# Performance work log

Measured on AMD Instinct MI355X. Metric: run time of the kernel, lower is better.

Reference implementation:

```python
import jax, jax.numpy as jnp
import numpy as np

N_EMBD = 1024
N_HEAD = 16
HEAD_DIM = N_EMBD // N_HEAD


def setup_inputs() -> dict:
    key = jax.random.key(0)
    ks = jax.random.split(key, 9)
    B, T, C = 2, 2048, N_EMBD
    s = 1.0 / np.sqrt(C)
    inp = {
        "x": jax.random.normal(ks[0], (B, T, C), dtype=jnp.float32),
        "Wq": jax.random.normal(ks[1], (C, C), dtype=jnp.float32) * s,
        "bq": jnp.zeros((C,), dtype=jnp.float32),
        "Wk": jax.random.normal(ks[2], (C, C), dtype=jnp.float32) * s,
        "bk": jnp.zeros((C,), dtype=jnp.float32),
        "Wv": jax.random.normal(ks[3], (C, C), dtype=jnp.float32) * s,
        "bv": jnp.zeros((C,), dtype=jnp.float32),
        "Wo": jax.random.normal(ks[4], (C, C), dtype=jnp.float32) * s,
        "bo": jnp.zeros((C,), dtype=jnp.float32),
    }
    return inp


def reference(x, Wq, bq, Wk, bk, Wv, bv, Wo, bo):
    B, T, C = x.shape
    H, D = N_HEAD, HEAD_DIM
    # projections (torch Linear: x @ W^T + b)
    q = (x @ Wq.T + bq).reshape(B, T, H, D).transpose(0, 2, 1, 3)  # [B,H,T,D]
    k = (x @ Wk.T + bk).reshape(B, T, H, D).transpose(0, 2, 1, 3)
    v = (x @ Wv.T + bv).reshape(B, T, H, D).transpose(0, 2, 1, 3)
    scores = jnp.einsum("bhqd,bhkd->bhqk", q, k) / jnp.sqrt(jnp.asarray(D, x.dtype))
    causal = jnp.tril(jnp.ones((T, T), dtype=bool))
    scores = jnp.where(causal[None, None], scores, jnp.asarray(-jnp.inf, x.dtype))
    weights = jax.nn.softmax(scores, axis=-1)  # [B,H,T,T]
    attended = jnp.einsum("bhqk,bhkd->bhqd", weights, v)
    attended = attended.transpose(0, 2, 1, 3).reshape(B, T, C)
    return attended @ Wo.T + bo
```

## Files before the change

kernel.cpp:

```cpp
#include <hip/hip_runtime.h>

typedef unsigned short u16;
typedef __attribute__((ext_vector_type(8))) __bf16 bf16x8;
typedef __attribute__((ext_vector_type(4))) float f32x4;
typedef __attribute__((ext_vector_type(4))) unsigned int u32x4;

#define MFMA16(a, b, c) __builtin_amdgcn_mfma_f32_16x16x32_bf16(a, b, c, 0, 0, 0)

__device__ __forceinline__ u16 f2bf(float f) {
    unsigned u = __float_as_uint(f);
    u = (u + 0x7FFFu + ((u >> 16) & 1u)) >> 16;
    return (u16)u;
}

__device__ __forceinline__ void gl_lds16(const u16* g, u16* l) {
    __builtin_amdgcn_global_load_lds(
        (const __attribute__((address_space(1))) unsigned int*)g,
        (__attribute__((address_space(3))) unsigned int*)l, 16, 0, 0);
}

static constexpr int Bv = 2, Tv = 2048, Cv = 1024, Hv = 16, Dv = 64;
static constexpr int Mv = Bv * Tv;

static constexpr size_t OFF_XB = 0;
static constexpr size_t OFF_WQ = 4194304;
static constexpr size_t OFF_WK = OFF_WQ + 1048576;
static constexpr size_t OFF_WV = OFF_WK + 1048576;
static constexpr size_t OFF_WO = OFF_WV + 1048576;
static constexpr size_t OFF_Q  = OFF_WO + 1048576;
static constexpr size_t OFF_K  = OFF_Q + 4194304;
static constexpr size_t OFF_VT = OFF_K + 4194304;
static constexpr size_t OFF_A  = OFF_VT + 4194304;

__global__ __launch_bounds__(256) void convert_all(
    const float* __restrict__ x,
    const float* __restrict__ wq, const float* __restrict__ wk,
    const float* __restrict__ wv, const float* __restrict__ wo,
    u16* __restrict__ dst)
{
    int i4 = blockIdx.x * blockDim.x + threadIdx.x;
    if (i4 >= 2097152) return;
    int idx = i4 * 4;
    const float* src; int off;
    if (idx < 4194304) { src = x; off = idx; }
    else {
        int rel = idx - 4194304;
        int j = rel >> 20;
        off = rel & 1048575;
        src = (j == 0) ? wq : (j == 1) ? wk : (j == 2) ? wv : wo;
    }
    float4 v = *(const float4*)(src + off);
    ushort4 o;
    o.x = f2bf(v.x); o.y = f2bf(v.y); o.z = f2bf(v.z); o.w = f2bf(v.w);
    *(ushort4*)(dst + idx) = o;
}

template <bool OUT_BF16, bool ROWBIAS>
__device__ __forceinline__ void gemm128_b64(
    u16* __restrict__ lA0, u16* __restrict__ lB0,
    u16* __restrict__ lA1, u16* __restrict__ lB1,
    const u16* __restrict__ A, const u16* __restrict__ Wt,
    const float* __restrict__ bias, void* __restrict__ outp,
    int m0, int n0, int N, int K)
{
    const int tid  = threadIdx.x;
    const int lane = tid & 63, w = tid >> 6;
    const int quad = lane >> 4, lm = lane & 15;
    const int wm = (w & 1) * 64, wn = (w >> 1) * 64;
    const int rowi = lane >> 3, seg = lane & 7;

    f32x4 zero = {0.f, 0.f, 0.f, 0.f};
    f32x4 acc[4][4];
    #pragma unroll
    for (int mt = 0; mt < 4; mt++)
        #pragma unroll
        for (int nt = 0; nt < 4; nt++) acc[mt][nt] = zero;

    auto stage = [&](u16* dA, u16* dB, int k0) __attribute__((always_inline)) {
        #pragma unroll
        for (int i = 0; i < 4; i++) {
            int rbase = w * 32 + i * 8;
            int row = rbase + rowi;
            int gseg = seg ^ (row & 7);
            gl_lds16(A  + (size_t)(m0 + row) * K + k0 + gseg * 8, &dA[rbase * 64]);
            gl_lds16(Wt + (size_t)(n0 + row) * K + k0 + gseg * 8, &dB[rbase * 64]);
        }
    };
    auto compute = [&](const u16* sA, const u16* sB) __attribute__((always_inline)) {
        #pragma unroll
        for (int ks = 0; ks < 2; ks++) {
            const int swz = ((ks * 4 + quad) ^ (lm & 7)) * 8;
            bf16x8 af[4], bf[4];
            #pragma unroll
            for (int mt = 0; mt < 4; mt++)
                af[mt] = *(const bf16x8*)&sA[(wm + mt * 16 + lm) * 64 + swz];
            #pragma unroll
            for (int nt = 0; nt < 4; nt++)
                bf[nt] = *(const bf16x8*)&sB[(wn + nt * 16 + lm) * 64 + swz];
            #pragma unroll
            for (int mt = 0; mt < 4; mt++)
                #pragma unroll
                for (int nt = 0; nt < 4; nt++)
                    acc[mt][nt] = MFMA16(af[mt], bf[nt], acc[mt][nt]);
        }
    };

    const int NT = K >> 6;
    stage(lA0, lB0, 0);
    __syncthreads();
    for (int t = 0; t < NT; t += 2) {
        if (t + 1 < NT) stage(lA1, lB1, (t + 1) << 6);
        compute(lA0, lB0);
        __syncthreads();
        if (t + 2 < NT) stage(lA0, lB0, (t + 2) << 6);
        if (t + 1 < NT) {
            compute(lA1, lB1);
            __syncthreads();
        }
    }

    #pragma unroll
    for (int nt = 0; nt < 4; nt++) {
        int col = n0 + wn + nt * 16 + lm;
        float cb = ROWBIAS ? 0.f : bias[col];
        #pragma unroll
        for (int mt = 0; mt < 4; mt++) {
            #pragma unroll
            for (int r = 0; r < 4; r++) {
                int row = m0 + wm + mt * 16 + quad * 4 + r;
                float v = acc[mt][nt][r] + (ROWBIAS ? bias[row] : cb);
                if (OUT_BF16) ((u16*)outp)[(size_t)row * N + col] = f2bf(v);
                else          ((float*)outp)[(size_t)row * N + col] = v;
            }
        }
    }
}

__global__ __launch_bounds__(256) void gemm_qkv(
    const u16* __restrict__ A,
    const u16* __restrict__ Wq, const u16* __restrict__ Wk, const u16* __restrict__ Wv,
    const float* __restrict__ bq, const float* __restrict__ bk, const float* __restrict__ bv,
    u16* __restrict__ Q, u16* __restrict__ K, u16* __restrict__ VT)
{
    __shared__ u16 lA0[128 * 64];
    __shared__ u16 lB0[128 * 64];
    __shared__ u16 lA1[128 * 64];
    __shared__ u16 lB1[128 * 64];

    int bid = blockIdx.x;
    int sw  = (bid & 7) * 96 + (bid >> 3);
    int g2  = sw >> 5;
    int row = sw & 31;
    int which = g2 >> 3, col = g2 & 7;

    if (which == 0) {
        gemm128_b64<true, false>(lA0, lB0, lA1, lB1, A, Wq, bq, Q, row * 128, col * 128, Cv, Cv);
    } else if (which == 1) {
        gemm128_b64<true, false>(lA0, lB0, lA1, lB1, A, Wk, bk, K, row * 128, col * 128, Cv, Cv);
    } else {
        gemm128_b64<true, true>(lA0, lB0, lA1, lB1, Wv, A, bv, VT, col * 128, row * 128, Mv, Cv);
    }
}

__global__ __launch_bounds__(256) void gemm_o64(
    const u16* __restrict__ A, const u16* __restrict__ Wt,
    const float* __restrict__ bias, float* __restrict__ outp)
{
    __shared__ u16 lA0[128 * 64];
    __shared__ u16 lA1[128 * 64];
    __shared__ u16 lB0[64 * 64];
    __shared__ u16 lB1[64 * 64];

    const int tid  = threadIdx.x;
    const int lane = tid & 63, w = tid >> 6;
    const int quad = lane >> 4, lm = lane & 15;

    int bid = blockIdx.x;
    int sw  = (bid & 7) * 64 + (bid >> 3);
    const int n0 = (sw >> 5) * 64;
    const int m0 = (sw & 31) * 128;
    const int K = Cv;
    const int rowi = lane >> 3, seg = lane & 7;

    f32x4 zero = {0.f, 0.f, 0.f, 0.f};
    f32x4 acc[2][4];
    #pragma unroll
    for (int mt = 0; mt < 2; mt++)
        #pragma unroll
        for (int nt = 0; nt < 4; nt++) acc[mt][nt] = zero;

    auto stage = [&](u16* dA, u16* dB, int k0) __attribute__((always_inline)) {
        #pragma unroll
        for (int i = 0; i < 4; i++) {
            int rbase = w * 32 + i * 8;
            int row = rbase + rowi;
            int gseg = seg ^ (row & 7);
            gl_lds16(A + (size_t)(m0 + row) * K + k0 + gseg * 8, &dA[rbase * 64]);
        }
        {
            int rbase = w * 16, row0 = rbase + rowi, row1 = row0 + 8;
            gl_lds16(Wt + (size_t)(n0 + row0) * K + k0 + (seg ^ (row0 & 7)) * 8, &dB[rbase * 64]);
            gl_lds16(Wt + (size_t)(n0 + row1) * K + k0 + (seg ^ (row1 & 7)) * 8, &dB[(rbase + 8) * 64]);
        }
    };
    auto compute = [&](const u16* sA, const u16* sB) __attribute__((always_inline)) {
        #pragma unroll
        for (int ks = 0; ks < 2; ks++) {
            const int swz = ((ks * 4 + quad) ^ (lm & 7)) * 8;
            bf16x8 af[2], bf[4];
            #pragma unroll
            for (int mt = 0; mt < 2; mt++)
                af[mt] = *(const bf16x8*)&sA[(w * 32 + mt * 16 + lm) * 64 + swz];
            #pragma unroll
            for (int nt = 0; nt < 4; nt++)
                bf[nt] = *(const bf16x8*)&sB[(nt * 16 + lm) * 64 + swz];
            #pragma unroll
            for (int mt = 0; mt < 2; mt++)
                #pragma unroll
                for (int nt = 0; nt < 4; nt++)
                    acc[mt][nt] = MFMA16(af[mt], bf[nt], acc[mt][nt]);
        }
    };

    const int NT = K >> 6;
    stage(lA0, lB0, 0);
    __syncthreads();
    for (int t = 0; t < NT; t += 2) {
        if (t + 1 < NT) stage(lA1, lB1, (t + 1) << 6);
        compute(lA0, lB0);
        __syncthreads();
        if (t + 2 < NT) stage(lA0, lB0, (t + 2) << 6);
        if (t + 1 < NT) {
            compute(lA1, lB1);
            __syncthreads();
        }
    }

    #pragma unroll
    for (int nt = 0; nt < 4; nt++) {
        int col = n0 + nt * 16 + lm;
        float bvv = bias[col];
        #pragma unroll
        for (int mt = 0; mt < 2; mt++) {
            #pragma unroll
            for (int r = 0; r < 4; r++) {
                int row = m0 + w * 32 + mt * 16 + quad * 4 + r;
                outp[(size_t)row * Cv + col] = acc[mt][nt][r] + bvv;
            }
        }
    }
}

__global__ __launch_bounds__(512) void attn(
    const u16* __restrict__ Qp, const u16* __restrict__ Kp,
    const u16* __restrict__ VTg, u16* __restrict__ Op)
{
    __shared__ u16 lK[2][64 * 64];
    __shared__ u16 lVT[2][64 * 64];
    __shared__ u16 lP[8][32][72];

    const int tid  = threadIdx.x;
    const int lane = tid & 63, w = tid >> 6;
    const int g = w >> 2, wl = w & 3;
    const int quad = lane >> 4, lm = lane & 15;

    const int idx  = blockIdx.x;
    const int half = idx >> 8;
    const int grp  = idx & 255;
    const int bh   = (half << 4) | (grp >> 4);
    const int j    = grp & 15;
    const int qt   = half ? j : 15 - j;
    const int h = bh & 15, b = bh >> 4;

    const int qb = qt * 128;
    const size_t headoff = (size_t)b * Tv * Cv + (size_t)h * Dv;
    const size_t vthead  = (size_t)h * 64 * Mv + (size_t)b * Tv;

    bf16x8 qf[2][2];
    #pragma unroll
    for (int nt = 0; nt < 2; nt++) {
        const u16* qptr = Qp + headoff + (size_t)(qb + wl * 32 + nt * 16 + lm) * Cv + quad * 8;
        qf[0][nt] = *(const bf16x8*)(qptr);
        qf[1][nt] = *(const bf16x8*)(qptr + 32);
    }

    f32x4 zero = {0.f, 0.f, 0.f, 0.f};
    f32x4 oacc[2][4];
    #pragma unroll
    for (int mt = 0; mt < 2; mt++)
        #pragma unroll
        for (int nt = 0; nt < 4; nt++) oacc[mt][nt] = zero;
    float Lp[2] = {0.f, 0.f};

    const float SC = 0.18033688011112042f;
    const int rowi = lane >> 3, seg = lane & 7;

    auto stage = [&](int kt) {
        const int k0 = kt * 64;
        #pragma unroll
        for (int hf = 0; hf < 2; hf++) {
            int rbase = wl * 16 + hf * 8;
            int row = rbase + rowi;
            int gseg = seg ^ (row & 7);
            gl_lds16(Kp + headoff + (size_t)(k0 + row) * Cv + gseg * 8, &lK[g][rbase * 64]);
            gl_lds16(VTg + vthead + (size_t)row * Mv + k0 + gseg * 8, &lVT[g][rbase * 64]);
        }
    };

    auto body = [&](int kt, bool domask) __attribute__((always_inline)) {
        const int k0 = kt * 64;
        f32x4 stt[4][2];
        #pragma unroll
        for (int mt = 0; mt < 4; mt++)
            #pragma unroll
            for (int nt = 0; nt < 2; nt++) stt[mt][nt] = zero;
        #pragma unroll
        for (int ks = 0; ks < 2; ks++) {
            #pragma unroll
            for (int mt = 0; mt < 4; mt++) {
                bf16x8 kf = *(const bf16x8*)
                    &lK[g][(mt * 16 + lm) * 64 + (((ks * 4 + quad) ^ (lm & 7)) * 8)];
                #pragma unroll
                for (int nt = 0; nt < 2; nt++)
                    stt[mt][nt] = MFMA16(kf, qf[ks][nt], stt[mt][nt]);
            }
        }
        #pragma unroll
        for (int mt = 0; mt < 4; mt++) {
            #pragma unroll
            for (int nt = 0; nt < 2; nt++) {
                const int keyb = k0 + mt * 16 + quad * 4;
                const int qrow = qb + wl * 32 + nt * 16 + lm;
                float e0 = __builtin_amdgcn_exp2f(fmaf(stt[mt][nt][0], SC, -16.f));
                float e1 = __builtin_amdgcn_exp2f(fmaf(stt[mt][nt][1], SC, -16.f));
                float e2 = __builtin_amdgcn_exp2f(fmaf(stt[mt][nt][2], SC, -16.f));
                float e3 = __builtin_amdgcn_exp2f(fmaf(stt[mt][nt][3], SC, -16.f));
                if (domask) {
                    if (keyb + 0 > qrow) e0 = 0.f;
                    if (keyb + 1 > qrow) e1 = 0.f;
                    if (keyb + 2 > qrow) e2 = 0.f;
                    if (keyb + 3 > qrow) e3 = 0.f;
                }
                Lp[nt] += e0 + e1 + e2 + e3;
                ushort4 pk;
                pk.x = (u16)(__float_as_uint(e0) >> 16);
                pk.y = (u16)(__float_as_uint(e1) >> 16);
                pk.z = (u16)(__float_as_uint(e2) >> 16);
                pk.w = (u16)(__float_as_uint(e3) >> 16);
                *(ushort4*)&lP[w][nt * 16 + lm][mt * 16 + quad * 4] = pk;
            }
        }
        #pragma unroll
        for (int ks = 0; ks < 2; ks++) {
            bf16x8 pf[2];
            #pragma unroll
            for (int mt = 0; mt < 2; mt++)
                pf[mt] = *(const bf16x8*)&lP[w][mt * 16 + lm][ks * 32 + quad * 8];
            #pragma unroll
            for (int nt = 0; nt < 4; nt++) {
                bf16x8 vf = *(const bf16x8*)
                    &lVT[g][(nt * 16 + lm) * 64 + (((ks * 4 + quad) ^ (lm & 7)) * 8)];
                #pragma unroll
                for (int mt = 0; mt < 2; mt++)
                    oacc[mt][nt] = MFMA16(pf[mt], vf, oacc[mt][nt]);
            }
        }
    };

    for (int i = 0; i < qt; i++) {
        if (i) __syncthreads();
        stage(2 * i + g);
        __syncthreads();
        body(2 * i + g, false);
    }
    if (qt) __syncthreads();
    stage(2 * qt + g);
    __syncthreads();
    body(2 * qt + g, true);
    __syncthreads();

    float* lO = (float*)&lP[0][0][0];
    float* lL = lO + 32 * 256;
    const int t = tid & 255;
    if (g == 1) {
        #pragma unroll
        for (int mt = 0; mt < 2; mt++)
            #pragma unroll
            for (int nt = 0; nt < 4; nt++)
                #pragma unroll
                for (int r = 0; r < 4; r++)
                    lO[(mt * 16 + nt * 4 + r) * 256 + t] = oacc[mt][nt][r];
        lL[t] = Lp[0];
        lL[256 + t] = Lp[1];
    }
    __syncthreads();
    if (g == 0) {
        #pragma unroll
        for (int mt = 0; mt < 2; mt++)
            #pragma unroll
            for (int nt = 0; nt < 4; nt++)
                #pragma unroll
                for (int r = 0; r < 4; r++)
                    oacc[mt][nt][r] += lO[(mt * 16 + nt * 4 + r) * 256 + t];
        Lp[0] += lL[t];
        Lp[1] += lL[256 + t];

        float Lred[2];
        #pragma unroll
        for (int nt = 0; nt < 2; nt++) {
            float L = Lp[nt];
            L += __shfl_xor(L, 16, 64);
            L += __shfl_xor(L, 32, 64);
            Lred[nt] = 1.0f / L;
        }
        #pragma unroll
        for (int mt = 0; mt < 2; mt++) {
            float inv[4];
            #pragma unroll
            for (int r = 0; r < 4; r++)
                inv[r] = __shfl(Lred[mt], (lane & 48) | (quad * 4 + r), 64);
            #pragma unroll
            for (int nt = 0; nt < 4; nt++) {
                #pragma unroll
                for (int r = 0; r < 4; r++) {
                    int row = qb + wl * 32 + mt * 16 + quad * 4 + r;
                    Op[headoff + (size_t)row * Cv + nt * 16 + lm] = f2bf(oacc[mt][nt][r] * inv[r]);
                }
            }
        }
    }
}

extern "C" void kernel_launch(void* const* d_in, const int* in_sizes, int n_in,
                              void* d_out, int out_size, void* d_ws, size_t ws_size,
                              hipStream_t stream) {
    const float* x  = (const float*)d_in[0];
    const float* Wq = (const float*)d_in[1];
    const float* bq = (const float*)d_in[2];
    const float* Wk = (const float*)d_in[3];
    const float* bk = (const float*)d_in[4];
    const float* Wv = (const float*)d_in[5];
    const float* bv = (const float*)d_in[6];
    const float* Wo = (const float*)d_in[7];
    const float* bo = (const float*)d_in[8];
    u16* ws = (u16*)d_ws;

    convert_all<<<8192, 256, 0, stream>>>(x, Wq, Wk, Wv, Wo, ws);

    gemm_qkv<<<768, 256, 0, stream>>>(
        ws + OFF_XB, ws + OFF_WQ, ws + OFF_WK, ws + OFF_WV,
        bq, bk, bv, ws + OFF_Q, ws + OFF_K, ws + OFF_VT);

    attn<<<512, 512, 0, stream>>>(ws + OFF_Q, ws + OFF_K, ws + OFF_VT, ws + OFF_A);

    gemm_o64<<<512, 256, 0, stream>>>(ws + OFF_A, ws + OFF_WO, bo, (float*)d_out);
}
```

Measured before the change: 182.3 us.

## Use partial vmcnt waits to keep two LDS stages in flight in GEMMs

Restructures the double-buffered GEMM main loops in both projection kernels. The next tile's global-to-LDS loads are now issued before the loop starts, and each iteration waits only until the current tile has landed, via s_waitcnt vmcnt with a nonzero count, instead of a full __syncthreads drain. This lets the load for tile t+1 overlap the compute of tile t. The risk is that the hardcoded vmcnt counts (8 and 6) must exactly match the number of loads each stage issues, or the kernel reads stale LDS data.

After: 182.6 us. About the same (+0.1%).

```diff
diff --git a/kernel.cpp b/kernel.cpp
--- a/kernel.cpp
+++ b/kernel.cpp
@@ -107,16 +107,17 @@
 
     const int NT = K >> 6;
     stage(lA0, lB0, 0);
-    __syncthreads();
-    for (int t = 0; t < NT; t += 2) {
-        if (t + 1 < NT) stage(lA1, lB1, (t + 1) << 6);
-        compute(lA0, lB0);
-        __syncthreads();
-        if (t + 2 < NT) stage(lA0, lB0, (t + 2) << 6);
-        if (t + 1 < NT) {
-            compute(lA1, lB1);
-            __syncthreads();
-        }
+    stage(lA1, lB1, 64);
+    for (int t = 0; t < NT; ++t) {
+        if (t + 1 < NT) asm volatile("s_waitcnt vmcnt(8)" ::: "memory");
+        else            asm volatile("s_waitcnt vmcnt(0)" ::: "memory");
+        __builtin_amdgcn_s_barrier();
+        u16* sA = (t & 1) ? lA1 : lA0;
+        u16* sB = (t & 1) ? lB1 : lB0;
+        compute(sA, sB);
+        asm volatile("s_waitcnt lgkmcnt(0)" ::: "memory");
+        __builtin_amdgcn_s_barrier();
+        if (t + 2 < NT) stage(sA, sB, (t + 2) << 6);
     }
 
     #pragma unroll
@@ -224,16 +225,17 @@
 
     const int NT = K >> 6;
     stage(lA0, lB0, 0);
-    __syncthreads();
-    for (int t = 0; t < NT; t += 2) {
-        if (t + 1 < NT) stage(lA1, lB1, (t + 1) << 6);
-        compute(lA0, lB0);
-        __syncthreads();
-        if (t + 2 < NT) stage(lA0, lB0, (t + 2) << 6);
-        if (t + 1 < NT) {
-            compute(lA1, lB1);
-            __syncthreads();
-        }
+    stage(lA1, lB1, 64);
+    for (int t = 0; t < NT; ++t) {
+        if (t + 1 < NT) asm volatile("s_waitcnt vmcnt(6)" ::: "memory");
+        else            asm volatile("s_waitcnt vmcnt(0)" ::: "memory");
+        __builtin_amdgcn_s_barrier();
+        u16* sA = (t & 1) ? lA1 : lA0;
+        u16* sB = (t & 1) ? lB1 : lB0;
+        compute(sA, sB);
+        asm volatile("s_waitcnt lgkmcnt(0)" ::: "memory");
+        __builtin_amdgcn_s_barrier();
+        if (t + 2 < NT) stage(sA, sB, (t + 2) << 6);
     }
 
     #pragma unroll
```
